# Optimization experiments

Hardware: AMD Instinct MI355X
Metric: run time of the kernel (lower is better)

Reference implementation:

```python
import jax, jax.numpy as jnp
import numpy as np
import math

IN_DIM = 2048
OUT_DIM = 1152
SEQ_LEN = 8
WAY = 5
SHOT = 5
N_QUERIES = 100
MAX_LEN = int(SEQ_LEN * 1.5)
PE_SCALE = 0.1


def make_pe():
    pe = np.zeros((MAX_LEN, IN_DIM), dtype=np.float32)
    position = np.arange(0, MAX_LEN)[:, None].astype(np.float32)
    div_term = np.exp(np.arange(0, IN_DIM, 2).astype(np.float32) * -(math.log(10000.0) / IN_DIM))
    pe[:, 0::2] = np.sin(position * div_term) * PE_SCALE
    pe[:, 1::2] = np.cos(position * div_term) * PE_SCALE
    return jnp.asarray(pe)


def setup_inputs() -> dict:
    key = jax.random.key(0)
    ks = jax.random.split(key, 12)
    support_set = jax.random.normal(ks[0], (WAY * SHOT, SEQ_LEN, IN_DIM), dtype=jnp.float32)
    queries = jax.random.normal(ks[1], (N_QUERIES, SEQ_LEN, IN_DIM), dtype=jnp.float32)
    # labels: each class 0..WAY-1 appears SHOT times (sorted)
    support_labels = jnp.sort(jnp.arange(WAY * SHOT) % WAY)
    s = 1.0 / math.sqrt(IN_DIM)
    def lin(k):
        kw, kb = jax.random.split(k)
        W = jax.random.uniform(kw, (OUT_DIM, IN_DIM), minval=-s, maxval=s, dtype=jnp.float32)
        b = jax.random.uniform(kb, (OUT_DIM,), minval=-s, maxval=s, dtype=jnp.float32)
        return W, b
    sk_W, sk_b = lin(ks[2])
    sv_W, sv_b = lin(ks[3])
    qk_W, qk_b = lin(ks[4])
    qv_W, qv_b = lin(ks[5])
    return {
        "support_set": support_set,
        "support_labels": support_labels,
        "queries": queries,
        "sk_W": sk_W, "sk_b": sk_b,
        "sv_W": sv_W, "sv_b": sv_b,
        "qk_W": qk_W, "qk_b": qk_b,
        "qv_W": qv_W, "qv_b": qv_b,
        "ln_k_g": jnp.ones((OUT_DIM,), jnp.float32),
        "ln_k_b": jnp.zeros((OUT_DIM,), jnp.float32),
        "pe_table": make_pe(),
    }


def layer_norm(x, g, b, eps=1e-5):
    mu = jnp.mean(x, axis=-1, keepdims=True)
    var = jnp.var(x, axis=-1, keepdims=True)
    return (x - mu) / jnp.sqrt(var + eps) * g + b


def reference(support_set, support_labels, queries, sk_W, sk_b, sv_W, sv_b,
              qk_W, qk_b, qv_W, qv_b, ln_k_g, ln_k_b, pe_table):
    n_q, L, _ = queries.shape
    support_set = support_set + pe_table[None, :L]
    queries = queries + pe_table[None, :L]

    s_ks = layer_norm(support_set @ sk_W.T + sk_b, ln_k_g, ln_k_b)  # [S, L, D]
    q_ks = layer_norm(queries @ qk_W.T + qk_b, ln_k_g, ln_k_b)      # [Q, L, D]
    s_vs = support_set @ sv_W.T + sv_b                               # [S, L, D]
    q_vs = queries @ qv_W.T + qv_b                                   # [Q, L, D]

    D = q_ks.shape[-1]
    # group support by class: labels are sorted with equal shots per class
    k_bs = support_set.shape[0] // WAY
    class_k = s_ks.reshape(WAY, k_bs, L, D)   # [C, k, L, D]
    class_v = s_vs.reshape(WAY, k_bs, L, D)

    # scores: [C, Q, L(query), k*L(support)]
    scores = jnp.einsum('qld,ckmd->cqlkm', q_ks, class_k) / math.sqrt(D)
    scores = scores.reshape(WAY, n_q, L, k_bs * L)
    attn = jax.nn.softmax(scores, axis=-1)  # softmax over support frames per query frame
    attn = attn.reshape(WAY, n_q, L, k_bs, L).transpose(0, 1, 3, 2, 4)  # [C,Q,k,L,L]
    proto = jnp.einsum('cqklm,ckmd->cqld', attn, class_v)  # sum over k folded in

    diff = q_vs[None] - proto  # [C, Q, L, D]
    distance = jnp.sum(diff * diff, axis=(-2, -1)) / math.sqrt(D * L)  # [C, Q]
    return -distance.T  # [Q, C]
```

## Files before the change

kernel.cpp:

```cpp
#include <hip/hip_runtime.h>
#include <hip/hip_bf16.h>
#include <math.h>

#define WAY     5
#define NQ      100
#define SEQL    8
#define IN_DIM  2048
#define OUT_DIM 1152
#define QROWS   800
#define SROWS   200
#define QPAD    896
#define SPAD    256

#define OFF_SKB  0
#define OFF_SVB  1152
#define OFF_QKB  2304
#define OFF_QVB  3456
#define OFF_LNG  4608
#define OFF_LNB  5760
#define OFF_RSQ  6912
#define F32_END  7808

#define U_AQ   0
#define U_AS   (U_AQ  + QPAD*IN_DIM)
#define U_QKB  (U_AS  + SPAD*IN_DIM)
#define U_QVB  (U_QKB + QPAD*OUT_DIM)
#define U_SKB  (U_QVB + QPAD*OUT_DIM)
#define U_SVB  (U_SKB + SPAD*OUT_DIM)
#define PPSZ   (2304*OUT_DIM)
#define U_PP   (U_SVB + SPAD*OUT_DIM)
#define SPSZ   (2048*SPAD)
#define U_SP   (U_PP + 4*PPSZ)
#define U_W    (U_SP + 4*SPSZ)

typedef __attribute__((ext_vector_type(8))) short short8;
typedef __attribute__((ext_vector_type(4))) float f32x4;

__device__ __forceinline__ float bf2f(unsigned short u) {
    return __uint_as_float(((unsigned int)u) << 16);
}
__device__ __forceinline__ unsigned short f2bf(float f) {
    unsigned int u = __float_as_uint(f);
    return (unsigned short)((u + 0x7fffu + ((u >> 16) & 1u)) >> 16);
}
__device__ __forceinline__ bool sniff_bf16(const void* lng) {
    return *((const unsigned int*)lng) != 0x3F800000u;
}
__device__ __forceinline__ float load_s(const void* p, long idx, bool bf) {
    if (bf) return bf2f(((const unsigned short*)p)[idx]);
    return ((const float*)p)[idx];
}
__device__ __forceinline__ float4 load_v4(const void* p, long idx, bool bf) {
    if (bf) {
        ushort4 v = *((const ushort4*)((const unsigned short*)p + idx));
        return make_float4(bf2f(v.x), bf2f(v.y), bf2f(v.z), bf2f(v.w));
    }
    return *((const float4*)((const float*)p + idx));
}
__device__ __forceinline__ void gl_lds16(const unsigned short* g, unsigned short* l) {
    __builtin_amdgcn_global_load_lds(
        (const __attribute__((address_space(1))) unsigned int*)g,
        (__attribute__((address_space(3))) unsigned int*)l,
        16, 0, 0);
}

__global__ void stage_kernel(const void* support, const void* queries,
                             const void* skW, const void* svW,
                             const void* qkW, const void* qvW,
                             const void* skb, const void* svb,
                             const void* qkb, const void* qvb,
                             const void* lng, const void* lnb,
                             const void* pe, float* ws) {
    const bool bf = sniff_bf16(lng);
    unsigned short* ub = (unsigned short*)(ws + F32_END);
    const int tid = blockIdx.x * blockDim.x + threadIdx.x;
    const int stride = gridDim.x * blockDim.x;

    for (int i = tid; i < OUT_DIM; i += stride) {
        ws[OFF_SKB + i] = load_s(skb, i, bf);
        ws[OFF_SVB + i] = load_s(svb, i, bf);
        ws[OFF_QKB + i] = load_s(qkb, i, bf);
        ws[OFF_QVB + i] = load_s(qvb, i, bf);
        ws[OFF_LNG + i] = load_s(lng, i, bf);
        ws[OFF_LNB + i] = load_s(lnb, i, bf);
    }
    for (int i = tid; i < QPAD * (IN_DIM / 4); i += stride) {
        const int row = i >> 9, kc = (i & 511) * 4;
        ushort4 o;
        if (row < QROWS) {
            float4 v = load_v4(queries, (long)row * IN_DIM + kc, bf);
            const float4 p = load_v4(pe, (long)(row & 7) * IN_DIM + kc, bf);
            o.x = f2bf(v.x + p.x); o.y = f2bf(v.y + p.y);
            o.z = f2bf(v.z + p.z); o.w = f2bf(v.w + p.w);
        } else o = make_ushort4(0, 0, 0, 0);
        *(ushort4*)&ub[U_AQ + (long)row * IN_DIM + kc] = o;
    }
    for (int i = tid; i < SPAD * (IN_DIM / 4); i += stride) {
        const int row = i >> 9, kc = (i & 511) * 4;
        ushort4 o;
        if (row < SROWS) {
            float4 v = load_v4(support, (long)row * IN_DIM + kc, bf);
            const float4 p = load_v4(pe, (long)(row & 7) * IN_DIM + kc, bf);
            o.x = f2bf(v.x + p.x); o.y = f2bf(v.y + p.y);
            o.z = f2bf(v.z + p.z); o.w = f2bf(v.w + p.w);
        } else o = make_ushort4(0, 0, 0, 0);
        *(ushort4*)&ub[U_AS + (long)row * IN_DIM + kc] = o;
    }
    if (!bf) {
        const float* Wsrc[4] = {(const float*)qkW, (const float*)qvW,
                                (const float*)skW, (const float*)svW};
        for (int j = 0; j < 4; ++j) {
            unsigned short* dst = ub + U_W + (long)j * OUT_DIM * IN_DIM;
            const float* src = Wsrc[j];
            for (int i = tid; i < OUT_DIM * (IN_DIM / 4); i += stride) {
                const long e = (long)i * 4;
                const float4 v = *(const float4*)(src + e);
                ushort4 o;
                o.x = f2bf(v.x); o.y = f2bf(v.y); o.z = f2bf(v.z); o.w = f2bf(v.w);
                *(ushort4*)&dst[e] = o;
            }
        }
    }
}

__global__ __launch_bounds__(256) void proj_mfma(
        const void* skW, const void* svW, const void* qkW, const void* qvW,
        const void* lng, float* ws) {
    const bool is_bf = sniff_bf16(lng);
    unsigned short* ub = (unsigned short*)(ws + F32_END);
    const int job = blockIdx.z >> 2;
    const int chunk = blockIdx.z & 3;
    if (job >= 4) return;
    if (job >= 2 && blockIdx.y >= 2) return;

    const unsigned short* A = (job < 2) ? (ub + U_AQ) : (ub + U_AS);
    const unsigned short* W;
    if (is_bf) {
        const void* Wp[4] = {qkW, qvW, skW, svW};
        W = (const unsigned short*)Wp[job];
    } else {
        W = ub + U_W + (size_t)job * OUT_DIM * IN_DIM;
    }
    const int rowbase[4] = {0, 896, 1792, 2048};
    unsigned short* out = ub + U_PP + (size_t)chunk * PPSZ
                        + (size_t)rowbase[job] * OUT_DIM;

    const int r0 = blockIdx.y * 128;
    const int n0 = blockIdx.x * 128;
    const int kbeg = chunk * 512;

    __shared__ unsigned short Als[128 * 32];
    __shared__ unsigned short Bls[128 * 32];

    const int t = threadIdx.x, w = t >> 6, l = t & 63;
    const int wr = w >> 1, wc = w & 1;
    const int fm = l & 15, fq = l >> 4;
    const int srow = l >> 2, schunk = (l & 3) * 8;

    const unsigned short* Ag = A + (size_t)(r0 + w * 32 + srow) * IN_DIM + schunk + kbeg;
    const unsigned short* Bg = W + (size_t)(n0 + w * 32 + srow) * IN_DIM + schunk + kbeg;
    unsigned short* Al0 = &Als[(w * 32) * 32];
    unsigned short* Al1 = &Als[(w * 32 + 16) * 32];
    unsigned short* Bl0 = &Bls[(w * 32) * 32];
    unsigned short* Bl1 = &Bls[(w * 32 + 16) * 32];

    f32x4 acc[4][4] = {};

    for (int k0 = 0; k0 < 512; k0 += 32) {
        __syncthreads();
        gl_lds16(Ag + k0, Al0);
        gl_lds16(Ag + (size_t)16 * IN_DIM + k0, Al1);
        gl_lds16(Bg + k0, Bl0);
        gl_lds16(Bg + (size_t)16 * IN_DIM + k0, Bl1);
        __syncthreads();

        short8 af[4], bff[4];
#pragma unroll
        for (int i = 0; i < 4; ++i)
            af[i] = *(const short8*)&Als[(wr * 64 + i * 16 + fm) * 32 + fq * 8];
#pragma unroll
        for (int j = 0; j < 4; ++j)
            bff[j] = *(const short8*)&Bls[(wc * 64 + j * 16 + fm) * 32 + fq * 8];
#pragma unroll
        for (int i = 0; i < 4; ++i)
#pragma unroll
            for (int j = 0; j < 4; ++j)
                acc[i][j] = __builtin_amdgcn_mfma_f32_16x16x32_bf16(
                    af[i], bff[j], acc[i][j], 0, 0, 0);
    }

#pragma unroll
    for (int j = 0; j < 4; ++j) {
        const int col = n0 + wc * 64 + j * 16 + fm;
#pragma unroll
        for (int i = 0; i < 4; ++i) {
            const int rb = r0 + wr * 64 + i * 16 + fq * 4;
            const f32x4 v = acc[i][j];
#pragma unroll
            for (int r = 0; r < 4; ++r)
                out[(size_t)(rb + r) * OUT_DIM + col] = f2bf(v[r]);
        }
    }
}

__global__ __launch_bounds__(256) void row_kernel(float* ws) {
    const int row = blockIdx.x;
    unsigned short* ub = (unsigned short*)(ws + F32_END);
    const unsigned short* pp = ub + U_PP + (size_t)row * OUT_DIM;
    const float* bias;
    unsigned short* outb;
    int mode, qrow = 0;
    if (row < 896)       { bias = ws + OFF_QKB; outb = ub + U_QKB + (size_t)row * OUT_DIM; mode = 0; }
    else if (row < 1792) { bias = ws + OFF_QVB; outb = ub + U_QVB + (size_t)(row - 896) * OUT_DIM; mode = 2; qrow = row - 896; }
    else if (row < 2048) { bias = ws + OFF_SKB; outb = ub + U_SKB + (size_t)(row - 1792) * OUT_DIM; mode = 0; }
    else                 { bias = ws + OFF_SVB; outb = ub + U_SVB + (size_t)(row - 2048) * OUT_DIM; mode = 1; }

    const int tid = threadIdx.x;
    __shared__ float red[4];
    __shared__ float xs[OUT_DIM];

    for (int i = tid; i < OUT_DIM / 8; i += 256) {
        float v[8];
        {
            const float4 b0 = *(const float4*)(bias + i * 8);
            const float4 b1 = *(const float4*)(bias + i * 8 + 4);
            v[0] = b0.x; v[1] = b0.y; v[2] = b0.z; v[3] = b0.w;
            v[4] = b1.x; v[5] = b1.y; v[6] = b1.z; v[7] = b1.w;
        }
#pragma unroll
        for (int p = 0; p < 4; ++p) {
            const short8 u = *(const short8*)(pp + (size_t)p * PPSZ + i * 8);
#pragma unroll
            for (int k = 0; k < 8; ++k) v[k] += bf2f((unsigned short)u[k]);
        }
#pragma unroll
        for (int k = 0; k < 8; ++k) xs[i * 8 + k] = v[k];
    }
    __syncthreads();

    if (mode == 0) {
        const float* g = ws + OFF_LNG;
        const float* bn = ws + OFF_LNB;
        float s = 0.f;
        for (int i = tid; i < OUT_DIM; i += 256) s += xs[i];
        for (int o = 32; o > 0; o >>= 1) s += __shfl_down(s, o, 64);
        if ((tid & 63) == 0) red[tid >> 6] = s;
        __syncthreads();
        const float mu = (red[0] + red[1] + red[2] + red[3]) * (1.0f / OUT_DIM);
        __syncthreads();
        float v = 0.f;
        for (int i = tid; i < OUT_DIM; i += 256) {
            float d = xs[i] - mu; v = fmaf(d, d, v);
        }
        for (int o = 32; o > 0; o >>= 1) v += __shfl_down(v, o, 64);
        if ((tid & 63) == 0) red[tid >> 6] = v;
        __syncthreads();
        const float var = (red[0] + red[1] + red[2] + red[3]) * (1.0f / OUT_DIM);
        const float rs = rsqrtf(var + 1e-5f);
        for (int i = tid; i < OUT_DIM; i += 256)
            outb[i] = f2bf((xs[i] - mu) * rs * g[i] + bn[i]);
    } else {
        float s = 0.f;
        for (int i = tid; i < OUT_DIM; i += 256) {
            const float v = xs[i];
            outb[i] = f2bf(v);
            s = fmaf(v, v, s);
        }
        if (mode == 2) {
            for (int o = 32; o > 0; o >>= 1) s += __shfl_down(s, o, 64);
            if ((tid & 63) == 0) red[tid >> 6] = s;
            __syncthreads();
            if (tid == 0) ws[OFF_RSQ + qrow] = red[0] + red[1] + red[2] + red[3];
        }
    }
}

__global__ __launch_bounds__(256) void pair_mfma(float* ws) {
    unsigned short* ub = (unsigned short*)(ws + F32_END);
    const int job = blockIdx.z >> 2;
    const int chunk = blockIdx.z & 3;
    if (job >= 3) return;
    if (job == 2 && blockIdx.y >= 4) return;

    const unsigned short* A;
    const unsigned short* B;
    int rowbase;
    if (job == 0)      { A = ub + U_QKB; B = ub + U_SKB; rowbase = 0; }
    else if (job == 1) { A = ub + U_QVB; B = ub + U_SVB; rowbase = 896; }
    else               { A = ub + U_SVB; B = ub + U_SVB; rowbase = 1792; }
    unsigned short* out = ub + U_SP + (size_t)chunk * SPSZ + (size_t)rowbase * SPAD;

    const int r0 = blockIdx.y * 64;
    const int n0 = blockIdx.x * 64;
    const int kbeg = chunk * 288;

    __shared__ unsigned short Als[64 * 32];
    __shared__ unsigned short Bls[64 * 32];

    const int t = threadIdx.x, w = t >> 6, l = t & 63;
    const int wr = w >> 1, wc = w & 1;
    const int fm = l & 15, fq = l >> 4;
    const int srow = l >> 2, schunk = (l & 3) * 8;

    const unsigned short* Ag = A + (size_t)(r0 + w * 16 + srow) * OUT_DIM + schunk + kbeg;
    const unsigned short* Bg = B + (size_t)(n0 + w * 16 + srow) * OUT_DIM + schunk + kbeg;
    unsigned short* Al = &Als[(w * 16) * 32];
    unsigned short* Bl = &Bls[(w * 16) * 32];

    f32x4 acc[2][2] = {};

    for (int k0 = 0; k0 < 288; k0 += 32) {
        __syncthreads();
        gl_lds16(Ag + k0, Al);
        gl_lds16(Bg + k0, Bl);
        __syncthreads();

        short8 af[2], bff[2];
#pragma unroll
        for (int i = 0; i < 2; ++i)
            af[i] = *(const short8*)&Als[(wr * 32 + i * 16 + fm) * 32 + fq * 8];
#pragma unroll
        for (int j = 0; j < 2; ++j)
            bff[j] = *(const short8*)&Bls[(wc * 32 + j * 16 + fm) * 32 + fq * 8];
#pragma unroll
        for (int i = 0; i < 2; ++i)
#pragma unroll
            for (int j = 0; j < 2; ++j)
                acc[i][j] = __builtin_amdgcn_mfma_f32_16x16x32_bf16(
                    af[i], bff[j], acc[i][j], 0, 0, 0);
    }

#pragma unroll
    for (int j = 0; j < 2; ++j) {
        const int col = n0 + wc * 32 + j * 16 + fm;
#pragma unroll
        for (int i = 0; i < 2; ++i) {
            const int rb = r0 + wr * 32 + i * 16 + fq * 4;
            const f32x4 v = acc[i][j];
#pragma unroll
            for (int r = 0; r < 4; ++r)
                out[(size_t)(rb + r) * SPAD + col] = f2bf(v[r]);
        }
    }
}

__global__ __launch_bounds__(256) void final_kernel(const void* lng, float* ws, void* outp) {
    const bool bf = sniff_bf16(lng);
    const int c = blockIdx.x;
    const int q = blockIdx.y;
    unsigned short* ub = (unsigned short*)(ws + F32_END);
    const unsigned short* P = ub + U_SP;

    __shared__ float sS[SEQL][40];
    __shared__ float sT[SEQL][40];
    __shared__ float sA[SEQL][40];
    __shared__ float sG[40][41];
    __shared__ float red[4];

    const int tid = threadIdx.x;
    const float isd = 0.029462782549439483f;

    for (int i = tid; i < SEQL * 40; i += 256) {
        const int l = i / 40, j = i % 40;
        const size_t rs = (size_t)(q * SEQL + l) * SPAD + c * 40 + j;
        const size_t rt = (size_t)(896 + q * SEQL + l) * SPAD + c * 40 + j;
        float s = 0.f, t = 0.f;
#pragma unroll
        for (int p = 0; p < 4; ++p) {
            s += bf2f(P[(size_t)p * SPSZ + rs]);
            t += bf2f(P[(size_t)p * SPSZ + rt]);
        }
        sS[l][j] = s * isd;
        sT[l][j] = t;
    }
    for (int i = tid; i < 40 * 40; i += 256) {
        const int j = i / 40, j2 = i % 40;
        const size_t rg = (size_t)(1792 + c * 40 + j) * SPAD + c * 40 + j2;
        float g = 0.f;
#pragma unroll
        for (int p = 0; p < 4; ++p) g += bf2f(P[(size_t)p * SPSZ + rg]);
        sG[j][j2] = g;
    }
    __syncthreads();

    if (tid < SEQL) {
        const int l = tid;
        float m = -1e30f;
        for (int j = 0; j < 40; ++j) m = fmaxf(m, sS[l][j]);
        float sum = 0.f;
        for (int j = 0; j < 40; ++j) { float e = __expf(sS[l][j] - m); sA[l][j] = e; sum += e; }
        const float inv = 1.0f / sum;
        for (int j = 0; j < 40; ++j) sA[l][j] *= inv;
    }
    __syncthreads();

    float part = 0.f;
    for (int i = tid; i < SEQL * 40; i += 256) {
        const int l = i / 40, j = i % 40;
        float gs = 0.f;
        for (int j2 = 0; j2 < 40; ++j2) gs = fmaf(sG[j][j2], sA[l][j2], gs);
        part += sA[l][j] * (gs - 2.0f * sT[l][j]);
    }
    for (int o = 32; o > 0; o >>= 1) part += __shfl_down(part, o, 64);
    if ((tid & 63) == 0) red[tid >> 6] = part;
    __syncthreads();

    if (tid == 0) {
        float qn = 0.f;
        for (int l = 0; l < SEQL; ++l) qn += ws[OFF_RSQ + q * SEQL + l];
        const float tot = red[0] + red[1] + red[2] + red[3] + qn;
        const float r = -(tot * (1.0f / 96.0f));
        if (bf) ((__hip_bfloat16*)outp)[q * WAY + c] = __float2bfloat16(r);
        else    ((float*)outp)[q * WAY + c] = r;
    }
}

extern "C" void kernel_launch(void* const* d_in, const int* in_sizes, int n_in,
                              void* d_out, int out_size, void* d_ws, size_t ws_size,
                              hipStream_t stream) {
    const void* support = d_in[0];
    const void* queries = d_in[2];
    const void* skW = d_in[3];  const void* skb = d_in[4];
    const void* svW = d_in[5];  const void* svb = d_in[6];
    const void* qkW = d_in[7];  const void* qkb = d_in[8];
    const void* qvW = d_in[9];  const void* qvb = d_in[10];
    const void* lng = d_in[11]; const void* lnb = d_in[12];
    const void* pe  = d_in[13];
    float* ws = (float*)d_ws;

    stage_kernel<<<dim3(512), dim3(256), 0, stream>>>(
        support, queries, skW, svW, qkW, qvW, skb, svb, qkb, qvb, lng, lnb, pe, ws);
    proj_mfma<<<dim3(9, 7, 16), dim3(256), 0, stream>>>(skW, svW, qkW, qvW, lng, ws);
    row_kernel<<<dim3(2304), dim3(256), 0, stream>>>(ws);
    pair_mfma<<<dim3(4, 14, 12), dim3(256), 0, stream>>>(ws);
    final_kernel<<<dim3(WAY, NQ), dim3(256), 0, stream>>>(lng, ws, d_out);
}
```

Before: 165.3 us.

## Fuse five phases into one persistent cooperative kernel with grid syncs

Merges the stage, projection GEMM, row-normalize, pair GEMM and final kernels into one persistent cooperative kernel. Blocks loop over the flattened work items and separate phases with grid.sync(), which removes four launch boundaries. If the cooperative launch fails, it falls back to the same phases as separate kernels. The grid is capped at 512 blocks, so phases with more work items than that (row with 2304, proj with 648) run several rounds per block, and grid-wide barriers add their own cost.

```diff
diff --git a/kernel.cpp b/kernel.cpp
--- a/kernel.cpp
+++ b/kernel.cpp
@@ -1,6 +1,9 @@
 #include <hip/hip_runtime.h>
 #include <hip/hip_bf16.h>
+#include <hip/hip_cooperative_groups.h>
 #include <math.h>
+
+namespace cg = cooperative_groups;
 
 #define WAY     5
 #define NQ      100
@@ -33,6 +36,8 @@
 #define U_SP   (U_PP + 4*PPSZ)
 #define U_W    (U_SP + 4*SPSZ)
 
+#define SMEM_BYTES 16384
+
 typedef __attribute__((ext_vector_type(8))) short short8;
 typedef __attribute__((ext_vector_type(4))) float f32x4;
 
@@ -64,17 +69,18 @@
         16, 0, 0);
 }
 
-__global__ void stage_kernel(const void* support, const void* queries,
-                             const void* skW, const void* svW,
-                             const void* qkW, const void* qvW,
-                             const void* skb, const void* svb,
-                             const void* qkb, const void* qvb,
-                             const void* lng, const void* lnb,
-                             const void* pe, float* ws) {
+__device__ __forceinline__ void ph_stage(
+        const void* support, const void* queries,
+        const void* skW, const void* svW,
+        const void* qkW, const void* qvW,
+        const void* skb, const void* svb,
+        const void* qkb, const void* qvb,
+        const void* lng, const void* lnb,
+        const void* pe, float* ws, int bid, int nblk) {
     const bool bf = sniff_bf16(lng);
     unsigned short* ub = (unsigned short*)(ws + F32_END);
-    const int tid = blockIdx.x * blockDim.x + threadIdx.x;
-    const int stride = gridDim.x * blockDim.x;
+    const int tid = bid * 256 + threadIdx.x;
+    const int stride = nblk * 256;
 
     for (int i = tid; i < OUT_DIM; i += stride) {
         ws[OFF_SKB + i] = load_s(skb, i, bf);
@@ -123,296 +129,349 @@
     }
 }
 
-__global__ __launch_bounds__(256) void proj_mfma(
+__device__ __forceinline__ void ph_proj(
         const void* skW, const void* svW, const void* qkW, const void* qvW,
-        const void* lng, float* ws) {
+        const void* lng, float* ws,
+        unsigned short* Als, unsigned short* Bls, int bid, int nblk) {
     const bool is_bf = sniff_bf16(lng);
     unsigned short* ub = (unsigned short*)(ws + F32_END);
-    const int job = blockIdx.z >> 2;
-    const int chunk = blockIdx.z & 3;
-    if (job >= 4) return;
-    if (job >= 2 && blockIdx.y >= 2) return;
-
-    const unsigned short* A = (job < 2) ? (ub + U_AQ) : (ub + U_AS);
-    const unsigned short* W;
-    if (is_bf) {
-        const void* Wp[4] = {qkW, qvW, skW, svW};
-        W = (const unsigned short*)Wp[job];
-    } else {
-        W = ub + U_W + (size_t)job * OUT_DIM * IN_DIM;
-    }
-    const int rowbase[4] = {0, 896, 1792, 2048};
-    unsigned short* out = ub + U_PP + (size_t)chunk * PPSZ
-                        + (size_t)rowbase[job] * OUT_DIM;
-
-    const int r0 = blockIdx.y * 128;
-    const int n0 = blockIdx.x * 128;
-    const int kbeg = chunk * 512;
-
-    __shared__ unsigned short Als[128 * 32];
-    __shared__ unsigned short Bls[128 * 32];
-
     const int t = threadIdx.x, w = t >> 6, l = t & 63;
     const int wr = w >> 1, wc = w & 1;
     const int fm = l & 15, fq = l >> 4;
     const int srow = l >> 2, schunk = (l & 3) * 8;
 
-    const unsigned short* Ag = A + (size_t)(r0 + w * 32 + srow) * IN_DIM + schunk + kbeg;
-    const unsigned short* Bg = W + (size_t)(n0 + w * 32 + srow) * IN_DIM + schunk + kbeg;
-    unsigned short* Al0 = &Als[(w * 32) * 32];
-    unsigned short* Al1 = &Als[(w * 32 + 16) * 32];
-    unsigned short* Bl0 = &Bls[(w * 32) * 32];
-    unsigned short* Bl1 = &Bls[(w * 32 + 16) * 32];
-
-    f32x4 acc[4][4] = {};
-
-    for (int k0 = 0; k0 < 512; k0 += 32) {
+    for (int jj = bid; jj < 648; jj += nblk) {
+        int job, nx, my, chunk;
+        if (jj < 504) { job = jj / 252; int r = jj % 252; nx = r % 9; my = (r / 9) % 7; chunk = r / 63; }
+        else          { int tt = jj - 504; job = 2 + tt / 72; int r = tt % 72; nx = r % 9; my = (r / 9) % 2; chunk = r / 18; }
+
+        const unsigned short* A = (job < 2) ? (ub + U_AQ) : (ub + U_AS);
+        const unsigned short* W;
+        if (is_bf) {
+            const void* Wv = (job == 0) ? qkW : (job == 1) ? qvW : (job == 2) ? skW : svW;
+            W = (const unsigned short*)Wv;
+        } else {
+            W = ub + U_W + (size_t)job * OUT_DIM * IN_DIM;
+        }
+        const int rb4 = (job == 0) ? 0 : (job == 1) ? 896 : (job == 2) ? 1792 : 2048;
+        unsigned short* out = ub + U_PP + (size_t)chunk * PPSZ + (size_t)rb4 * OUT_DIM;
+
+        const int r0 = my * 128;
+        const int n0 = nx * 128;
+        const int kbeg = chunk * 512;
+
+        const unsigned short* Ag = A + (size_t)(r0 + w * 32 + srow) * IN_DIM + schunk + kbeg;
+        const unsigned short* Bg = W + (size_t)(n0 + w * 32 + srow) * IN_DIM + schunk + kbeg;
+        unsigned short* Al0 = &Als[(w * 32) * 32];
+        unsigned short* Al1 = &Als[(w * 32 + 16) * 32];
+        unsigned short* Bl0 = &Bls[(w * 32) * 32];
+        unsigned short* Bl1 = &Bls[(w * 32 + 16) * 32];
+
+        f32x4 acc[4][4] = {};
+
+        for (int k0 = 0; k0 < 512; k0 += 32) {
+            __syncthreads();
+            gl_lds16(Ag + k0, Al0);
+            gl_lds16(Ag + (size_t)16 * IN_DIM + k0, Al1);
+            gl_lds16(Bg + k0, Bl0);
+            gl_lds16(Bg + (size_t)16 * IN_DIM + k0, Bl1);
+            __syncthreads();
+
+            short8 af[4], bff[4];
+#pragma unroll
+            for (int i = 0; i < 4; ++i)
+                af[i] = *(const short8*)&Als[(wr * 64 + i * 16 + fm) * 32 + fq * 8];
+#pragma unroll
+            for (int j = 0; j < 4; ++j)
+                bff[j] = *(const short8*)&Bls[(wc * 64 + j * 16 + fm) * 32 + fq * 8];
+#pragma unroll
+            for (int i = 0; i < 4; ++i)
+#pragma unroll
+                for (int j = 0; j < 4; ++j)
+                    acc[i][j] = __builtin_amdgcn_mfma_f32_16x16x32_bf16(
+                        af[i], bff[j], acc[i][j], 0, 0, 0);
+        }
+
+#pragma unroll
+        for (int j = 0; j < 4; ++j) {
+            const int col = n0 + wc * 64 + j * 16 + fm;
+#pragma unroll
+            for (int i = 0; i < 4; ++i) {
+                const int rb = r0 + wr * 64 + i * 16 + fq * 4;
+                const f32x4 v = acc[i][j];
+#pragma unroll
+                for (int r = 0; r < 4; ++r)
+                    out[(size_t)(rb + r) * OUT_DIM + col] = f2bf(v[r]);
+            }
+        }
+    }
+}
+
+__device__ __forceinline__ void ph_row(float* ws, float* xs, float* red,
+                                       int bid, int nblk) {
+    unsigned short* ub = (unsigned short*)(ws + F32_END);
+    const int tid = threadIdx.x;
+
+    for (int row = bid; row < 2304; row += nblk) {
+        const unsigned short* pp = ub + U_PP + (size_t)row * OUT_DIM;
+        const float* bias;
+        unsigned short* outb;
+        int mode, qrow = 0;
+        if (row < 896)       { bias = ws + OFF_QKB; outb = ub + U_QKB + (size_t)row * OUT_DIM; mode = 0; }
+        else if (row < 1792) { bias = ws + OFF_QVB; outb = ub + U_QVB + (size_t)(row - 896) * OUT_DIM; mode = 2; qrow = row - 896; }
+        else if (row < 2048) { bias = ws + OFF_SKB; outb = ub + U_SKB + (size_t)(row - 1792) * OUT_DIM; mode = 0; }
+        else                 { bias = ws + OFF_SVB; outb = ub + U_SVB + (size_t)(row - 2048) * OUT_DIM; mode = 1; }
+
+        for (int i = tid; i < OUT_DIM / 8; i += 256) {
+            float v[8];
+            {
+                const float4 b0 = *(const float4*)(bias + i * 8);
+                const float4 b1 = *(const float4*)(bias + i * 8 + 4);
+                v[0] = b0.x; v[1] = b0.y; v[2] = b0.z; v[3] = b0.w;
+                v[4] = b1.x; v[5] = b1.y; v[6] = b1.z; v[7] = b1.w;
+            }
+#pragma unroll
+            for (int p = 0; p < 4; ++p) {
+                const short8 u = *(const short8*)(pp + (size_t)p * PPSZ + i * 8);
+#pragma unroll
+                for (int k = 0; k < 8; ++k) v[k] += bf2f((unsigned short)u[k]);
+            }
+#pragma unroll
+            for (int k = 0; k < 8; ++k) xs[i * 8 + k] = v[k];
+        }
         __syncthreads();
-        gl_lds16(Ag + k0, Al0);
-        gl_lds16(Ag + (size_t)16 * IN_DIM + k0, Al1);
-        gl_lds16(Bg + k0, Bl0);
-        gl_lds16(Bg + (size_t)16 * IN_DIM + k0, Bl1);
-        __syncthreads();
-
-        short8 af[4], bff[4];
-#pragma unroll
-        for (int i = 0; i < 4; ++i)
-            af[i] = *(const short8*)&Als[(wr * 64 + i * 16 + fm) * 32 + fq * 8];
-#pragma unroll
-        for (int j = 0; j < 4; ++j)
-            bff[j] = *(const short8*)&Bls[(wc * 64 + j * 16 + fm) * 32 + fq * 8];
-#pragma unroll
-        for (int i = 0; i < 4; ++i)
-#pragma unroll
-            for (int j = 0; j < 4; ++j)
-                acc[i][j] = __builtin_amdgcn_mfma_f32_16x16x32_bf16(
-                    af[i], bff[j], acc[i][j], 0, 0, 0);
-    }
-
-#pragma unroll
-    for (int j = 0; j < 4; ++j) {
-        const int col = n0 + wc * 64 + j * 16 + fm;
-#pragma unroll
-        for (int i = 0; i < 4; ++i) {
-            const int rb = r0 + wr * 64 + i * 16 + fq * 4;
-            const f32x4 v = acc[i][j];
-#pragma unroll
-            for (int r = 0; r < 4; ++r)
-                out[(size_t)(rb + r) * OUT_DIM + col] = f2bf(v[r]);
-        }
-    }
-}
-
-__global__ __launch_bounds__(256) void row_kernel(float* ws) {
-    const int row = blockIdx.x;
-    unsigned short* ub = (unsigned short*)(ws + F32_END);
-    const unsigned short* pp = ub + U_PP + (size_t)row * OUT_DIM;
-    const float* bias;
-    unsigned short* outb;
-    int mode, qrow = 0;
-    if (row < 896)       { bias = ws + OFF_QKB; outb = ub + U_QKB + (size_t)row * OUT_DIM; mode = 0; }
-    else if (row < 1792) { bias = ws + OFF_QVB; outb = ub + U_QVB + (size_t)(row - 896) * OUT_DIM; mode = 2; qrow = row - 896; }
-    else if (row < 2048) { bias = ws + OFF_SKB; outb = ub + U_SKB + (size_t)(row - 1792) * OUT_DIM; mode = 0; }
-    else                 { bias = ws + OFF_SVB; outb = ub + U_SVB + (size_t)(row - 2048) * OUT_DIM; mode = 1; }
-
-    const int tid = threadIdx.x;
-    __shared__ float red[4];
-    __shared__ float xs[OUT_DIM];
-
-    for (int i = tid; i < OUT_DIM / 8; i += 256) {
-        float v[8];
-        {
-            const float4 b0 = *(const float4*)(bias + i * 8);
-            const float4 b1 = *(const float4*)(bias + i * 8 + 4);
-            v[0] = b0.x; v[1] = b0.y; v[2] = b0.z; v[3] = b0.w;
-            v[4] = b1.x; v[5] = b1.y; v[6] = b1.z; v[7] = b1.w;
-        }
-#pragma unroll
-        for (int p = 0; p < 4; ++p) {
-            const short8 u = *(const short8*)(pp + (size_t)p * PPSZ + i * 8);
-#pragma unroll
-            for (int k = 0; k < 8; ++k) v[k] += bf2f((unsigned short)u[k]);
-        }
-#pragma unroll
-        for (int k = 0; k < 8; ++k) xs[i * 8 + k] = v[k];
-    }
-    __syncthreads();
-
-    if (mode == 0) {
-        const float* g = ws + OFF_LNG;
-        const float* bn = ws + OFF_LNB;
-        float s = 0.f;
-        for (int i = tid; i < OUT_DIM; i += 256) s += xs[i];
-        for (int o = 32; o > 0; o >>= 1) s += __shfl_down(s, o, 64);
-        if ((tid & 63) == 0) red[tid >> 6] = s;
-        __syncthreads();
-        const float mu = (red[0] + red[1] + red[2] + red[3]) * (1.0f / OUT_DIM);
-        __syncthreads();
-        float v = 0.f;
-        for (int i = tid; i < OUT_DIM; i += 256) {
-            float d = xs[i] - mu; v = fmaf(d, d, v);
-        }
-        for (int o = 32; o > 0; o >>= 1) v += __shfl_down(v, o, 64);
-        if ((tid & 63) == 0) red[tid >> 6] = v;
-        __syncthreads();
-        const float var = (red[0] + red[1] + red[2] + red[3]) * (1.0f / OUT_DIM);
-        const float rs = rsqrtf(var + 1e-5f);
-        for (int i = tid; i < OUT_DIM; i += 256)
-            outb[i] = f2bf((xs[i] - mu) * rs * g[i] + bn[i]);
-    } else {
-        float s = 0.f;
-        for (int i = tid; i < OUT_DIM; i += 256) {
-            const float v = xs[i];
-            outb[i] = f2bf(v);
-            s = fmaf(v, v, s);
-        }
-        if (mode == 2) {
+
+        if (mode == 0) {
+            const float* g = ws + OFF_LNG;
+            const float* bn = ws + OFF_LNB;
+            float s = 0.f;
+            for (int i = tid; i < OUT_DIM; i += 256) s += xs[i];
             for (int o = 32; o > 0; o >>= 1) s += __shfl_down(s, o, 64);
             if ((tid & 63) == 0) red[tid >> 6] = s;
             __syncthreads();
-            if (tid == 0) ws[OFF_RSQ + qrow] = red[0] + red[1] + red[2] + red[3];
-        }
-    }
-}
-
-__global__ __launch_bounds__(256) void pair_mfma(float* ws) {
+            const float mu = (red[0] + red[1] + red[2] + red[3]) * (1.0f / OUT_DIM);
+            __syncthreads();
+            float v = 0.f;
+            for (int i = tid; i < OUT_DIM; i += 256) {
+                float d = xs[i] - mu; v = fmaf(d, d, v);
+            }
+            for (int o = 32; o > 0; o >>= 1) v += __shfl_down(v, o, 64);
+            if ((tid & 63) == 0) red[tid >> 6] = v;
+            __syncthreads();
+            const float var = (red[0] + red[1] + red[2] + red[3]) * (1.0f / OUT_DIM);
+            const float rs = rsqrtf(var + 1e-5f);
+            for (int i = tid; i < OUT_DIM; i += 256)
+                outb[i] = f2bf((xs[i] - mu) * rs * g[i] + bn[i]);
+        } else {
+            float s = 0.f;
+            for (int i = tid; i < OUT_DIM; i += 256) {
+                const float v = xs[i];
+                outb[i] = f2bf(v);
+                s = fmaf(v, v, s);
+            }
+            if (mode == 2) {
+                for (int o = 32; o > 0; o >>= 1) s += __shfl_down(s, o, 64);
+                if ((tid & 63) == 0) red[tid >> 6] = s;
+                __syncthreads();
+                if (tid == 0) ws[OFF_RSQ + qrow] = red[0] + red[1] + red[2] + red[3];
+            }
+        }
+        __syncthreads();
+    }
+}
+
+__device__ __forceinline__ void ph_pair(float* ws, unsigned short* Als,
+                                        unsigned short* Bls, int bid, int nblk) {
     unsigned short* ub = (unsigned short*)(ws + F32_END);
-    const int job = blockIdx.z >> 2;
-    const int chunk = blockIdx.z & 3;
-    if (job >= 3) return;
-    if (job == 2 && blockIdx.y >= 4) return;
-
-    const unsigned short* A;
-    const unsigned short* B;
-    int rowbase;
-    if (job == 0)      { A = ub + U_QKB; B = ub + U_SKB; rowbase = 0; }
-    else if (job == 1) { A = ub + U_QVB; B = ub + U_SVB; rowbase = 896; }
-    else               { A = ub + U_SVB; B = ub + U_SVB; rowbase = 1792; }
-    unsigned short* out = ub + U_SP + (size_t)chunk * SPSZ + (size_t)rowbase * SPAD;
-
-    const int r0 = blockIdx.y * 64;
-    const int n0 = blockIdx.x * 64;
-    const int kbeg = chunk * 288;
-
-    __shared__ unsigned short Als[64 * 32];
-    __shared__ unsigned short Bls[64 * 32];
-
     const int t = threadIdx.x, w = t >> 6, l = t & 63;
     const int wr = w >> 1, wc = w & 1;
     const int fm = l & 15, fq = l >> 4;
     const int srow = l >> 2, schunk = (l & 3) * 8;
 
-    const unsigned short* Ag = A + (size_t)(r0 + w * 16 + srow) * OUT_DIM + schunk + kbeg;
-    const unsigned short* Bg = B + (size_t)(n0 + w * 16 + srow) * OUT_DIM + schunk + kbeg;
-    unsigned short* Al = &Als[(w * 16) * 32];
-    unsigned short* Bl = &Bls[(w * 16) * 32];
-
-    f32x4 acc[2][2] = {};
-
-    for (int k0 = 0; k0 < 288; k0 += 32) {
-        __syncthreads();
-        gl_lds16(Ag + k0, Al);
-        gl_lds16(Bg + k0, Bl);
-        __syncthreads();
-
-        short8 af[2], bff[2];
-#pragma unroll
-        for (int i = 0; i < 2; ++i)
-            af[i] = *(const short8*)&Als[(wr * 32 + i * 16 + fm) * 32 + fq * 8];
-#pragma unroll
-        for (int j = 0; j < 2; ++j)
-            bff[j] = *(const short8*)&Bls[(wc * 32 + j * 16 + fm) * 32 + fq * 8];
-#pragma unroll
-        for (int i = 0; i < 2; ++i)
+    for (int jj = bid; jj < 512; jj += nblk) {
+        int job, nx, my, chunk;
+        if (jj < 448) { job = jj / 224; int r = jj % 224; nx = r % 4; my = (r / 4) % 14; chunk = r / 56; }
+        else          { int tt = jj - 448; job = 2; nx = tt % 4; my = (tt / 4) % 4; chunk = tt / 16; }
+
+        const unsigned short* A;
+        const unsigned short* B;
+        int rowbase;
+        if (job == 0)      { A = ub + U_QKB; B = ub + U_SKB; rowbase = 0; }
+        else if (job == 1) { A = ub + U_QVB; B = ub + U_SVB; rowbase = 896; }
+        else               { A = ub + U_SVB; B = ub + U_SVB; rowbase = 1792; }
+        unsigned short* out = ub + U_SP + (size_t)chunk * SPSZ + (size_t)rowbase * SPAD;
+
+        const int r0 = my * 64;
+        const int n0 = nx * 64;
+        const int kbeg = chunk * 288;
+
+        const unsigned short* Ag = A + (size_t)(r0 + w * 16 + srow) * OUT_DIM + schunk + kbeg;
+        const unsigned short* Bg = B + (size_t)(n0 + w * 16 + srow) * OUT_DIM + schunk + kbeg;
+        unsigned short* Al = &Als[(w * 16) * 32];
+        unsigned short* Bl = &Bls[(w * 16) * 32];
+
+        f32x4 acc[2][2] = {};
+
+        for (int k0 = 0; k0 < 288; k0 += 32) {
+            __syncthreads();
+            gl_lds16(Ag + k0, Al);
+            gl_lds16(Bg + k0, Bl);
+            __syncthreads();
+
+            short8 af[2], bff[2];
+#pragma unroll
+            for (int i = 0; i < 2; ++i)
+                af[i] = *(const short8*)&Als[(wr * 32 + i * 16 + fm) * 32 + fq * 8];
 #pragma unroll
             for (int j = 0; j < 2; ++j)
-                acc[i][j] = __builtin_amdgcn_mfma_f32_16x16x32_bf16(
-                    af[i], bff[j], acc[i][j], 0, 0, 0);
-    }
-
-#pragma unroll
-    for (int j = 0; j < 2; ++j) {
-        const int col = n0 + wc * 32 + j * 16 + fm;
-#pragma unroll
-        for (int i = 0; i < 2; ++i) {
-            const int rb = r0 + wr * 32 + i * 16 + fq * 4;
-            const f32x4 v = acc[i][j];
-#pragma unroll
-            for (int r = 0; r < 4; ++r)
-                out[(size_t)(rb + r) * SPAD + col] = f2bf(v[r]);
-        }
-    }
-}
-
-__global__ __launch_bounds__(256) void final_kernel(const void* lng, float* ws, void* outp) {
+                bff[j] = *(const short8*)&Bls[(wc * 32 + j * 16 + fm) * 32 + fq * 8];
+#pragma unroll
+            for (int i = 0; i < 2; ++i)
+#pragma unroll
+                for (int j = 0; j < 2; ++j)
+                    acc[i][j] = __builtin_amdgcn_mfma_f32_16x16x32_bf16(
+                        af[i], bff[j], acc[i][j], 0, 0, 0);
+        }
+
+#pragma unroll
+        for (int j = 0; j < 2; ++j) {
+            const int col = n0 + wc * 32 + j * 16 + fm;
+#pragma unroll
+            for (int i = 0; i < 2; ++i) {
+                const int rb = r0 + wr * 32 + i * 16 + fq * 4;
+                const f32x4 v = acc[i][j];
+#pragma unroll
+                for (int r = 0; r < 4; ++r)
+                    out[(size_t)(rb + r) * SPAD + col] = f2bf(v[r]);
+            }
+        }
+    }
+}
+
+__device__ __forceinline__ void ph_final(const void* lng, float* ws, void* outp,
+                                         float* smf, int bid, int nblk) {
     const bool bf = sniff_bf16(lng);
-    const int c = blockIdx.x;
-    const int q = blockIdx.y;
     unsigned short* ub = (unsigned short*)(ws + F32_END);
     const unsigned short* P = ub + U_SP;
 
-    __shared__ float sS[SEQL][40];
-    __shared__ float sT[SEQL][40];
-    __shared__ float sA[SEQL][40];
-    __shared__ float sG[40][41];
-    __shared__ float red[4];
+    float* sS  = smf;
+    float* sT  = smf + 320;
+    float* sA  = smf + 640;
+    float* sG  = smf + 960;
+    float* red = smf + 2600;
 
     const int tid = threadIdx.x;
     const float isd = 0.029462782549439483f;
 
-    for (int i = tid; i < SEQL * 40; i += 256) {
-        const int l = i / 40, j = i % 40;
-        const size_t rs = (size_t)(q * SEQL + l) * SPAD + c * 40 + j;
-        const size_t rt = (size_t)(896 + q * SEQL + l) * SPAD + c * 40 + j;
-        float s = 0.f, t = 0.f;
-#pragma unroll
-        for (int p = 0; p < 4; ++p) {
-            s += bf2f(P[(size_t)p * SPSZ + rs]);
-            t += bf2f(P[(size_t)p * SPSZ + rt]);
-        }
-        sS[l][j] = s * isd;
-        sT[l][j] = t;
-    }
-    for (int i = tid; i < 40 * 40; i += 256) {
-        const int j = i / 40, j2 = i % 40;
-        const size_t rg = (size_t)(1792 + c * 40 + j) * SPAD + c * 40 + j2;
-        float g = 0.f;
-#pragma unroll
-        for (int p = 0; p < 4; ++p) g += bf2f(P[(size_t)p * SPSZ + rg]);
-        sG[j][j2] = g;
-    }
-    __syncthreads();
-
-    if (tid < SEQL) {
-        const int l = tid;
-        float m = -1e30f;
-        for (int j = 0; j < 40; ++j) m = fmaxf(m, sS[l][j]);
-        float sum = 0.f;
-        for (int j = 0; j < 40; ++j) { float e = __expf(sS[l][j] - m); sA[l][j] = e; sum += e; }
-        const float inv = 1.0f / sum;
-        for (int j = 0; j < 40; ++j) sA[l][j] *= inv;
-    }
-    __syncthreads();
-
-    float part = 0.f;
-    for (int i = tid; i < SEQL * 40; i += 256) {
-        const int l = i / 40, j = i % 40;
-        float gs = 0.f;
-        for (int j2 = 0; j2 < 40; ++j2) gs = fmaf(sG[j][j2], sA[l][j2], gs);
-        part += sA[l][j] * (gs - 2.0f * sT[l][j]);
-    }
-    for (int o = 32; o > 0; o >>= 1) part += __shfl_down(part, o, 64);
-    if ((tid & 63) == 0) red[tid >> 6] = part;
-    __syncthreads();
-
-    if (tid == 0) {
-        float qn = 0.f;
-        for (int l = 0; l < SEQL; ++l) qn += ws[OFF_RSQ + q * SEQL + l];
-        const float tot = red[0] + red[1] + red[2] + red[3] + qn;
-        const float r = -(tot * (1.0f / 96.0f));
-        if (bf) ((__hip_bfloat16*)outp)[q * WAY + c] = __float2bfloat16(r);
-        else    ((float*)outp)[q * WAY + c] = r;
-    }
+    for (int jj = bid; jj < 500; jj += nblk) {
+        const int c = jj / 100, q = jj - c * 100;
+
+        for (int i = tid; i < SEQL * 40; i += 256) {
+            const int l = i / 40, j = i % 40;
+            const size_t rs = (size_t)(q * SEQL + l) * SPAD + c * 40 + j;
+            const size_t rt = (size_t)(896 + q * SEQL + l) * SPAD + c * 40 + j;
+            float s = 0.f, t2 = 0.f;
+#pragma unroll
+            for (int p = 0; p < 4; ++p) {
+                s  += bf2f(P[(size_t)p * SPSZ + rs]);
+                t2 += bf2f(P[(size_t)p * SPSZ + rt]);
+            }
+            sS[l * 40 + j] = s * isd;
+            sT[l * 40 + j] = t2;
+        }
+        for (int i = tid; i < 40 * 40; i += 256) {
+            const int j = i / 40, j2 = i % 40;
+            const size_t rg = (size_t)(1792 + c * 40 + j) * SPAD + c * 40 + j2;
+            float g = 0.f;
+#pragma unroll
+            for (int p = 0; p < 4; ++p) g += bf2f(P[(size_t)p * SPSZ + rg]);
+            sG[j * 41 + j2] = g;
+        }
+        __syncthreads();
+
+        if (tid < SEQL) {
+            const int l = tid;
+            float m = -1e30f;
+            for (int j = 0; j < 40; ++j) m = fmaxf(m, sS[l * 40 + j]);
+            float sum = 0.f;
+            for (int j = 0; j < 40; ++j) { float e = __expf(sS[l * 40 + j] - m); sA[l * 40 + j] = e; sum += e; }
+            const float inv = 1.0f / sum;
+            for (int j = 0; j < 40; ++j) sA[l * 40 + j] *= inv;
+        }
+        __syncthreads();
+
+        float part = 0.f;
+        for (int i = tid; i < SEQL * 40; i += 256) {
+            const int l = i / 40, j = i % 40;
+            float gs = 0.f;
+            for (int j2 = 0; j2 < 40; ++j2) gs = fmaf(sG[j * 41 + j2], sA[l * 40 + j2], gs);
+            part += sA[l * 40 + j] * (gs - 2.0f * sT[l * 40 + j]);
+        }
+        for (int o = 32; o > 0; o >>= 1) part += __shfl_down(part, o, 64);
+        if ((tid & 63) == 0) red[tid >> 6] = part;
+        __syncthreads();
+
+        if (tid == 0) {
+            float qn = 0.f;
+            for (int l = 0; l < SEQL; ++l) qn += ws[OFF_RSQ + q * SEQL + l];
+            const float tot = red[0] + red[1] + red[2] + red[3] + qn;
+            const float r = -(tot * (1.0f / 96.0f));
+            if (bf) ((__hip_bfloat16*)outp)[q * WAY + c] = __float2bfloat16(r);
+            else    ((float*)outp)[q * WAY + c] = r;
+        }
+        __syncthreads();
+    }
+}
+
+__global__ __launch_bounds__(256, 2) void mega(
+        const void* support, const void* queries,
+        const void* skW, const void* svW, const void* qkW, const void* qvW,
+        const void* skb, const void* svb, const void* qkb, const void* qvb,
+        const void* lng, const void* lnb, const void* pe,
+        float* ws, void* outp) {
+    __shared__ __align__(16) unsigned char smem[SMEM_BYTES];
+    cg::grid_group grid = cg::this_grid();
+    const int bid = blockIdx.x, nblk = gridDim.x;
+
+    ph_stage(support, queries, skW, svW, qkW, qvW, skb, svb, qkb, qvb,
+             lng, lnb, pe, ws, bid, nblk);
+    grid.sync();
+    ph_proj(skW, svW, qkW, qvW, lng, ws,
+            (unsigned short*)smem, (unsigned short*)(smem + 8192), bid, nblk);
+    grid.sync();
+    ph_row(ws, (float*)smem, (float*)(smem + 4608), bid, nblk);
+    grid.sync();
+    ph_pair(ws, (unsigned short*)smem, (unsigned short*)(smem + 4096), bid, nblk);
+    grid.sync();
+    ph_final(lng, ws, outp, (float*)smem, bid, nblk);
+}
+
+__global__ __launch_bounds__(256) void k_stage(
+        const void* support, const void* queries,
+        const void* skW, const void* svW, const void* qkW, const void* qvW,
+        const void* skb, const void* svb, const void* qkb, const void* qvb,
+        const void* lng, const void* lnb, const void* pe, float* ws) {
+    ph_stage(support, queries, skW, svW, qkW, qvW, skb, svb, qkb, qvb,
+             lng, lnb, pe, ws, blockIdx.x, gridDim.x);
+}
+__global__ __launch_bounds__(256) void k_proj(
+        const void* skW, const void* svW, const void* qkW, const void* qvW,
+        const void* lng, float* ws) {
+    __shared__ __align__(16) unsigned char sm[SMEM_BYTES];
+    ph_proj(skW, svW, qkW, qvW, lng, ws,
+            (unsigned short*)sm, (unsigned short*)(sm + 8192), blockIdx.x, gridDim.x);
+}
+__global__ __launch_bounds__(256) void k_row(float* ws) {
+    __shared__ __align__(16) unsigned char sm[SMEM_BYTES];
+    ph_row(ws, (float*)sm, (float*)(sm + 4608), blockIdx.x, gridDim.x);
+}
+__global__ __launch_bounds__(256) void k_pair(float* ws) {
+    __shared__ __align__(16) unsigned char sm[SMEM_BYTES];
+    ph_pair(ws, (unsigned short*)sm, (unsigned short*)(sm + 4096), blockIdx.x, gridDim.x);
+}
+__global__ __launch_bounds__(256) void k_final(const void* lng, float* ws, void* outp) {
+    __shared__ __align__(16) unsigned char sm[SMEM_BYTES];
+    ph_final(lng, ws, outp, (float*)sm, blockIdx.x, gridDim.x);
 }
 
 extern "C" void kernel_launch(void* const* d_in, const int* in_sizes, int n_in,
@@ -427,11 +486,31 @@
     const void* lng = d_in[11]; const void* lnb = d_in[12];
     const void* pe  = d_in[13];
     float* ws = (float*)d_ws;
-
-    stage_kernel<<<dim3(512), dim3(256), 0, stream>>>(
-        support, queries, skW, svW, qkW, qvW, skb, svb, qkb, qvb, lng, lnb, pe, ws);
-    proj_mfma<<<dim3(9, 7, 16), dim3(256), 0, stream>>>(skW, svW, qkW, qvW, lng, ws);
-    row_kernel<<<dim3(2304), dim3(256), 0, stream>>>(ws);
-    pair_mfma<<<dim3(4, 14, 12), dim3(256), 0, stream>>>(ws);
-    final_kernel<<<dim3(WAY, NQ), dim3(256), 0, stream>>>(lng, ws, d_out);
-}
+    void* outp = d_out;
+
+    static int gblocks = 0;
+    if (gblocks == 0) {
+        int nb = 0;
+        if (hipOccupancyMaxActiveBlocksPerMultiprocessor(&nb, mega, 256, 0) != hipSuccess || nb < 1)
+            nb = 1;
+        gblocks = nb * 256;
+        if (gblocks > 512) gblocks = 512;
+    }
+
+    void* args[] = {(void*)&support, (void*)&queries,
+                    (void*)&skW, (void*)&svW, (void*)&qkW, (void*)&qvW,
+                    (void*)&skb, (void*)&svb, (void*)&qkb, (void*)&qvb,
+                    (void*)&lng, (void*)&lnb, (void*)&pe,
+                    (void*)&ws, (void*)&outp};
+    hipError_t err = hipLaunchCooperativeKernel(
+        mega, dim3(gblocks), dim3(256), args, 0u, stream);
+
+    if (err != hipSuccess) {
+        k_stage<<<dim3(512), dim3(256), 0, stream>>>(
+            support, queries, skW, svW, qkW, qvW, skb, svb, qkb, qvb, lng, lnb, pe, ws);
+        k_proj<<<dim3(648), dim3(256), 0, stream>>>(skW, svW, qkW, qvW, lng, ws);
+        k_row<<<dim3(2304), dim3(256), 0, stream>>>(ws);
+        k_pair<<<dim3(512), dim3(256), 0, stream>>>(ws);
+        k_final<<<dim3(500), dim3(256), 0, stream>>>(lng, ws, d_out);
+    }
+}
```

After: 357.0 us. 116% more time.

## Double-buffer LDS tiles in GEMM kernels and fuse layernorm statistics into one pass

Applied to the files above, without the earlier changes.

Both MFMA GEMM kernels now use two LDS buffers per operand. The next k-tile's global-to-LDS load is issued before the current tile's MFMAs, and the loop needs one barrier per step instead of two. The row kernel computes the sum and sum of squares in the same pass that accumulates partials, and the value rows write bf16 output directly. This removes extra passes and barriers but uses the E[x^2]-mu^2 variance form, which can lose precision, and doubles LDS use.

```diff
diff --git a/kernel.cpp b/kernel.cpp
--- a/kernel.cpp
+++ b/kernel.cpp
@@ -149,8 +149,8 @@
     const int n0 = blockIdx.x * 128;
     const int kbeg = chunk * 512;
 
-    __shared__ unsigned short Als[128 * 32];
-    __shared__ unsigned short Bls[128 * 32];
+    __shared__ unsigned short Als[2][128 * 32];
+    __shared__ unsigned short Bls[2][128 * 32];
 
     const int t = threadIdx.x, w = t >> 6, l = t & 63;
     const int wr = w >> 1, wc = w & 1;
@@ -159,34 +159,43 @@
 
     const unsigned short* Ag = A + (size_t)(r0 + w * 32 + srow) * IN_DIM + schunk + kbeg;
     const unsigned short* Bg = W + (size_t)(n0 + w * 32 + srow) * IN_DIM + schunk + kbeg;
-    unsigned short* Al0 = &Als[(w * 32) * 32];
-    unsigned short* Al1 = &Als[(w * 32 + 16) * 32];
-    unsigned short* Bl0 = &Bls[(w * 32) * 32];
-    unsigned short* Bl1 = &Bls[(w * 32 + 16) * 32];
+    const int l0 = (w * 32) * 32;
+    const int l1 = (w * 32 + 16) * 32;
 
     f32x4 acc[4][4] = {};
 
+    gl_lds16(Ag, &Als[0][l0]);
+    gl_lds16(Ag + (size_t)16 * IN_DIM, &Als[0][l1]);
+    gl_lds16(Bg, &Bls[0][l0]);
+    gl_lds16(Bg + (size_t)16 * IN_DIM, &Bls[0][l1]);
+    __syncthreads();
+
+    int cur = 0;
     for (int k0 = 0; k0 < 512; k0 += 32) {
-        __syncthreads();
-        gl_lds16(Ag + k0, Al0);
-        gl_lds16(Ag + (size_t)16 * IN_DIM + k0, Al1);
-        gl_lds16(Bg + k0, Bl0);
-        gl_lds16(Bg + (size_t)16 * IN_DIM + k0, Bl1);
-        __syncthreads();
+        const int nxt = cur ^ 1;
+        if (k0 + 32 < 512) {
+            gl_lds16(Ag + k0 + 32, &Als[nxt][l0]);
+            gl_lds16(Ag + (size_t)16 * IN_DIM + k0 + 32, &Als[nxt][l1]);
+            gl_lds16(Bg + k0 + 32, &Bls[nxt][l0]);
+            gl_lds16(Bg + (size_t)16 * IN_DIM + k0 + 32, &Bls[nxt][l1]);
+        }
 
         short8 af[4], bff[4];
 #pragma unroll
         for (int i = 0; i < 4; ++i)
-            af[i] = *(const short8*)&Als[(wr * 64 + i * 16 + fm) * 32 + fq * 8];
+            af[i] = *(const short8*)&Als[cur][(wr * 64 + i * 16 + fm) * 32 + fq * 8];
 #pragma unroll
         for (int j = 0; j < 4; ++j)
-            bff[j] = *(const short8*)&Bls[(wc * 64 + j * 16 + fm) * 32 + fq * 8];
+            bff[j] = *(const short8*)&Bls[cur][(wc * 64 + j * 16 + fm) * 32 + fq * 8];
 #pragma unroll
         for (int i = 0; i < 4; ++i)
 #pragma unroll
             for (int j = 0; j < 4; ++j)
                 acc[i][j] = __builtin_amdgcn_mfma_f32_16x16x32_bf16(
                     af[i], bff[j], acc[i][j], 0, 0, 0);
+
+        __syncthreads();
+        cur = nxt;
     }
 
 #pragma unroll
@@ -216,9 +225,10 @@
     else                 { bias = ws + OFF_SVB; outb = ub + U_SVB + (size_t)(row - 2048) * OUT_DIM; mode = 1; }
 
     const int tid = threadIdx.x;
-    __shared__ float red[4];
+    __shared__ float red[8];
     __shared__ float xs[OUT_DIM];
 
+    float s = 0.f, s2 = 0.f;
     for (int i = tid; i < OUT_DIM / 8; i += 256) {
         float v[8];
         {
@@ -233,45 +243,43 @@
 #pragma unroll
             for (int k = 0; k < 8; ++k) v[k] += bf2f((unsigned short)u[k]);
         }
-#pragma unroll
-        for (int k = 0; k < 8; ++k) xs[i * 8 + k] = v[k];
-    }
-    __syncthreads();
+        if (mode == 0) {
+#pragma unroll
+            for (int k = 0; k < 8; ++k) {
+                xs[i * 8 + k] = v[k];
+                s += v[k];
+                s2 = fmaf(v[k], v[k], s2);
+            }
+        } else {
+#pragma unroll
+            for (int k = 0; k < 8; ++k) {
+                outb[i * 8 + k] = f2bf(v[k]);
+                s2 = fmaf(v[k], v[k], s2);
+            }
+        }
+    }
 
     if (mode == 0) {
+        for (int o = 32; o > 0; o >>= 1) {
+            s  += __shfl_down(s,  o, 64);
+            s2 += __shfl_down(s2, o, 64);
+        }
+        if ((tid & 63) == 0) { red[tid >> 6] = s; red[4 + (tid >> 6)] = s2; }
+        __syncthreads();
+        const float S  = red[0] + red[1] + red[2] + red[3];
+        const float S2 = red[4] + red[5] + red[6] + red[7];
+        const float mu = S * (1.0f / OUT_DIM);
+        const float var = S2 * (1.0f / OUT_DIM) - mu * mu;
+        const float rs = rsqrtf(var + 1e-5f);
         const float* g = ws + OFF_LNG;
         const float* bn = ws + OFF_LNB;
-        float s = 0.f;
-        for (int i = tid; i < OUT_DIM; i += 256) s += xs[i];
-        for (int o = 32; o > 0; o >>= 1) s += __shfl_down(s, o, 64);
-        if ((tid & 63) == 0) red[tid >> 6] = s;
-        __syncthreads();
-        const float mu = (red[0] + red[1] + red[2] + red[3]) * (1.0f / OUT_DIM);
-        __syncthreads();
-        float v = 0.f;
-        for (int i = tid; i < OUT_DIM; i += 256) {
-            float d = xs[i] - mu; v = fmaf(d, d, v);
-        }
-        for (int o = 32; o > 0; o >>= 1) v += __shfl_down(v, o, 64);
-        if ((tid & 63) == 0) red[tid >> 6] = v;
-        __syncthreads();
-        const float var = (red[0] + red[1] + red[2] + red[3]) * (1.0f / OUT_DIM);
-        const float rs = rsqrtf(var + 1e-5f);
         for (int i = tid; i < OUT_DIM; i += 256)
             outb[i] = f2bf((xs[i] - mu) * rs * g[i] + bn[i]);
-    } else {
-        float s = 0.f;
-        for (int i = tid; i < OUT_DIM; i += 256) {
-            const float v = xs[i];
-            outb[i] = f2bf(v);
-            s = fmaf(v, v, s);
-        }
-        if (mode == 2) {
-            for (int o = 32; o > 0; o >>= 1) s += __shfl_down(s, o, 64);
-            if ((tid & 63) == 0) red[tid >> 6] = s;
-            __syncthreads();
-            if (tid == 0) ws[OFF_RSQ + qrow] = red[0] + red[1] + red[2] + red[3];
-        }
+    } else if (mode == 2) {
+        for (int o = 32; o > 0; o >>= 1) s2 += __shfl_down(s2, o, 64);
+        if ((tid & 63) == 0) red[tid >> 6] = s2;
+        __syncthreads();
+        if (tid == 0) ws[OFF_RSQ + qrow] = red[0] + red[1] + red[2] + red[3];
     }
 }
 
@@ -294,8 +302,8 @@
     const int n0 = blockIdx.x * 64;
     const int kbeg = chunk * 288;
 
-    __shared__ unsigned short Als[64 * 32];
-    __shared__ unsigned short Bls[64 * 32];
+    __shared__ unsigned short Als[2][64 * 32];
+    __shared__ unsigned short Bls[2][64 * 32];
 
     const int t = threadIdx.x, w = t >> 6, l = t & 63;
     const int wr = w >> 1, wc = w & 1;
@@ -304,30 +312,38 @@
 
     const unsigned short* Ag = A + (size_t)(r0 + w * 16 + srow) * OUT_DIM + schunk + kbeg;
     const unsigned short* Bg = B + (size_t)(n0 + w * 16 + srow) * OUT_DIM + schunk + kbeg;
-    unsigned short* Al = &Als[(w * 16) * 32];
-    unsigned short* Bl = &Bls[(w * 16) * 32];
+    const int lofs = (w * 16) * 32;
 
     f32x4 acc[2][2] = {};
 
+    gl_lds16(Ag, &Als[0][lofs]);
+    gl_lds16(Bg, &Bls[0][lofs]);
+    __syncthreads();
+
+    int cur = 0;
     for (int k0 = 0; k0 < 288; k0 += 32) {
-        __syncthreads();
-        gl_lds16(Ag + k0, Al);
-        gl_lds16(Bg + k0, Bl);
-        __syncthreads();
+        const int nxt = cur ^ 1;
+        if (k0 + 32 < 288) {
+            gl_lds16(Ag + k0 + 32, &Als[nxt][lofs]);
+            gl_lds16(Bg + k0 + 32, &Bls[nxt][lofs]);
+        }
 
         short8 af[2], bff[2];
 #pragma unroll
         for (int i = 0; i < 2; ++i)
-            af[i] = *(const short8*)&Als[(wr * 32 + i * 16 + fm) * 32 + fq * 8];
+            af[i] = *(const short8*)&Als[cur][(wr * 32 + i * 16 + fm) * 32 + fq * 8];
 #pragma unroll
         for (int j = 0; j < 2; ++j)
-            bff[j] = *(const short8*)&Bls[(wc * 32 + j * 16 + fm) * 32 + fq * 8];
+            bff[j] = *(const short8*)&Bls[cur][(wc * 32 + j * 16 + fm) * 32 + fq * 8];
 #pragma unroll
         for (int i = 0; i < 2; ++i)
 #pragma unroll
             for (int j = 0; j < 2; ++j)
                 acc[i][j] = __builtin_amdgcn_mfma_f32_16x16x32_bf16(
                     af[i], bff[j], acc[i][j], 0, 0, 0);
+
+        __syncthreads();
+        cur = nxt;
     }
 
 #pragma unroll
```

After: 165.3 us. No clear change (+0.1%).
